# Performance work log

Measured on AMD Instinct MI355X. Metric: run time of the kernel, lower is better.

The kernel has to match this reference:

```python
import jax, jax.numpy as jnp
import numpy as np

B, S, D = 1, 2048, 1024
H, DK = 16, 64
DFF, E, K = 4096, 8, 2
EPS = float(np.finfo(np.float32).eps)  # torch nn.RMSNorm default eps = finfo.eps


def setup_inputs() -> dict:
    key = jax.random.key(0)
    ks = jax.random.split(key, 8)
    s = 0.02
    return {
        "x": jax.random.normal(ks[0], (B, S, D), jnp.float32),
        "qkv_w": jax.random.normal(ks[1], (3 * D, D), jnp.float32) * s,
        "out_w": jax.random.normal(ks[2], (D, D), jnp.float32) * s,
        "router_w": jax.random.normal(ks[3], (E, D), jnp.float32) * s,
        "w1": jax.random.normal(ks[4], (E, DFF, D), jnp.float32) * s,
        "w2": jax.random.normal(ks[5], (E, D, DFF), jnp.float32) * s,
        "norm1_w": jnp.ones((D,), jnp.float32),
        "norm2_w": jnp.ones((D,), jnp.float32),
    }


def _rmsnorm(x, w):
    return x * jax.lax.rsqrt(jnp.mean(x * x, axis=-1, keepdims=True) + EPS) * w


def _rope(x):
    # x: [B, S, H, dk]; rotate-half RoPE as in RotaryPositionalEmbedding
    dk = x.shape[-1]
    inv_freq = 1.0 / (10000.0 ** (jnp.arange(0, dk, 2, dtype=jnp.float32) / dk))
    t = jnp.arange(x.shape[1], dtype=jnp.float32)
    freqs = t[:, None] * inv_freq[None, :]          # [S, dk/2]
    cos = jnp.cos(freqs)[None, :, None, :]
    sin = jnp.sin(freqs)[None, :, None, :]
    x1, x2 = jnp.split(x, 2, axis=-1)
    return jnp.concatenate([x1 * cos - x2 * sin, x2 * cos + x1 * sin], axis=-1)


def _block(x, qkv_w, out_w, router_w, w1, w2, norm1_w, norm2_w):
    Bv, Sv, Dv = x.shape
    # --- attention with RoPE (causal, eval mode) ---
    h = _rmsnorm(x, norm1_w)
    qkv = (h @ qkv_w.T).reshape(Bv, Sv, 3, H, DK)
    q, k, v = qkv[:, :, 0], qkv[:, :, 1], qkv[:, :, 2]   # [B,S,H,dk]
    q = _rope(q)
    k = _rope(k)
    scores = jnp.einsum('bshd,bthd->bhst', q, k) / np.float32(np.sqrt(DK))
    causal = jnp.tril(jnp.ones((Sv, Sv), dtype=bool))
    scores = jnp.where(causal, scores, jnp.float32(-jnp.inf))
    attn = jax.nn.softmax(scores, axis=-1)
    o = jnp.einsum('bhst,bthd->bshd', attn, v).reshape(Bv, Sv, Dv)
    x = x + o @ out_w.T
    # --- MoE with top-k routing ---
    h2 = _rmsnorm(x, norm2_w).reshape(-1, Dv)            # [T, D]
    logits = h2 @ router_w.T                             # [T, E]
    probs = jax.nn.softmax(logits, axis=-1)
    top_p, top_i = jax.lax.top_k(probs, K)               # [T, K]
    top_p = top_p / jnp.sum(top_p, axis=-1, keepdims=True)
    T = h2.shape[0]
    # dense per-token per-expert combine weights (same math as masked loop)
    w_dense = jnp.zeros((T, E), h2.dtype).at[jnp.arange(T)[:, None], top_i].add(top_p)
    hid = jax.nn.gelu(jnp.einsum('td,efd->etf', h2, w1), approximate=False)  # [E,T,DFF]
    eo = jnp.einsum('etf,edf->etd', hid, w2)                                  # [E,T,D]
    moe = jnp.einsum('etd,te->td', eo, w_dense).reshape(Bv, Sv, Dv)
    aux_loss = E * jnp.sum(jnp.mean(probs, axis=0) ** 2)
    return x + moe, aux_loss


def reference(x, qkv_w, out_w, router_w, w1, w2, norm1_w, norm2_w):
    return _block(x, qkv_w, out_w, router_w, w1, w2, norm1_w, norm2_w)
```

## Files before the change

### kernel.cpp

```cpp
#include <hip/hip_runtime.h>
#include <cstdint>
#include <math.h>

typedef float f32x4 __attribute__((ext_vector_type(4)));
typedef __bf16 bf16x8 __attribute__((ext_vector_type(8)));
typedef unsigned short us4 __attribute__((ext_vector_type(4)));
typedef unsigned short us8 __attribute__((ext_vector_type(8)));

#define DEV static __device__ __forceinline__

DEV unsigned short f2bf(float f){
  union { __bf16 h; unsigned short u; } cv; cv.h = (__bf16)f; return cv.u;
}
DEV float bf2f(unsigned short u){ return __uint_as_float((unsigned int)u << 16); }

DEV void gload16(const void* g, void* l){
  __builtin_amdgcn_global_load_lds((__attribute__((address_space(1))) void*)g,
                                   (__attribute__((address_space(3))) void*)l, 16, 0, 0);
}

__global__ __launch_bounds__(256) void conv_kernel(const float* __restrict__ src,
    unsigned short* __restrict__ dst, int n8){
  int i = blockIdx.x*256 + threadIdx.x;
  if (i >= n8) return;
  float4 a = ((const float4*)src)[2*i];
  float4 b = ((const float4*)src)[2*i+1];
  us8 o = { f2bf(a.x), f2bf(a.y), f2bf(a.z), f2bf(a.w),
            f2bf(b.x), f2bf(b.y), f2bf(b.z), f2bf(b.w) };
  ((us8*)dst)[i] = o;
}

__global__ __launch_bounds__(256) void rmsnorm_kernel(const float* __restrict__ x, const float* __restrict__ w,
    unsigned short* __restrict__ ob){
  int t = blockIdx.x, tid = threadIdx.x;
  float4 xv = *(const float4*)(x + (long long)t*1024 + tid*4);
  float ss = xv.x*xv.x + xv.y*xv.y + xv.z*xv.z + xv.w*xv.w;
  for (int m=32;m;m>>=1) ss += __shfl_xor(ss,m);
  __shared__ float lds[4];
  if ((tid&63)==0) lds[tid>>6] = ss;
  __syncthreads();
  float tot = lds[0]+lds[1]+lds[2]+lds[3];
  float inv = rsqrtf(tot*(1.0f/1024.0f) + 1.1920928955078125e-07f);
  float4 wv = *(const float4*)(w + tid*4);
  us4 rb = { f2bf(xv.x*inv*wv.x), f2bf(xv.y*inv*wv.y), f2bf(xv.z*inv*wv.z), f2bf(xv.w*inv*wv.w) };
  *(us4*)&ob[(long long)t*1024 + tid*4] = rb;
}

__global__ __launch_bounds__(256) void rmsnorm2_kernel(const float* __restrict__ xp, int ksn, long long kstride,
    const float* __restrict__ w, float* __restrict__ x1, unsigned short* __restrict__ hb, float* __restrict__ hf){
  int t = blockIdx.x, tid = threadIdx.x;
  long long b = (long long)t*1024 + tid*4;
  float4 xv = {0.f,0.f,0.f,0.f};
  for (int ks=0; ks<ksn; ++ks){
    float4 a = *(const float4*)(xp + ks*kstride + b);
    xv.x+=a.x; xv.y+=a.y; xv.z+=a.z; xv.w+=a.w;
  }
  *(float4*)(x1 + b) = xv;
  float ss = xv.x*xv.x + xv.y*xv.y + xv.z*xv.z + xv.w*xv.w;
  for (int m=32;m;m>>=1) ss += __shfl_xor(ss,m);
  __shared__ float lds[4];
  if ((tid&63)==0) lds[tid>>6] = ss;
  __syncthreads();
  float tot = lds[0]+lds[1]+lds[2]+lds[3];
  float inv = rsqrtf(tot*(1.0f/1024.0f) + 1.1920928955078125e-07f);
  float4 wv = *(const float4*)(w + tid*4);
  float r0 = xv.x*inv*wv.x, r1 = xv.y*inv*wv.y, r2 = xv.z*inv*wv.z, r3 = xv.w*inv*wv.w;
  us4 rb = { f2bf(r0), f2bf(r1), f2bf(r2), f2bf(r3) };
  *(us4*)&hb[b] = rb;
  float4 rf; rf.x=r0; rf.y=r1; rf.z=r2; rf.w=r3;
  *(float4*)(hf + b) = rf;
}

template<int EPI, bool GATHER>
__global__ __launch_bounds__(256) void gemm_bb(
    const unsigned short* __restrict__ A, int lda,
    const unsigned short* __restrict__ Bb, long long bstride, int ldb,
    int M, int N, int K, int KS, long long ksoff,
    const int* __restrict__ counts, const int* __restrict__ offs,
    const int* __restrict__ tok_list, const float* __restrict__ wgt,
    const float* __restrict__ resid,
    float* __restrict__ Cf, unsigned short* __restrict__ Cb, int ldc)
{
  const int z = blockIdx.z;
  const int e = z / KS, ks = z - e*KS;
  const int Me = counts ? counts[e] : M;
  const int by = blockIdx.y;
  if (by * 128 >= Me) return;
  const int rbase = offs ? offs[e] : 0;
  const int bx = blockIdx.x;
  const unsigned short* B = Bb + (long long)e * bstride;
  const int kn = K / KS;
  const int kbeg = ks * kn;

  __shared__ __align__(16) unsigned short As[128*64];
  __shared__ __align__(16) unsigned short Bs[128*64];

  const int tid = threadIdx.x, lane = tid & 63, w = tid >> 6;
  const int wr = w >> 1, wc = w & 1;
  const int l15 = lane & 15, l4 = lane >> 4;

  const unsigned short* asrc[4];
  const unsigned short* bsrc[4];
  #pragma unroll
  for (int j=0;j<4;++j){
    int G = j*256 + tid;
    int R = G >> 3, c = G & 7;
    int sc = c ^ (R & 7);
    int lr = by*128 + R; if (lr >= Me) lr = Me-1;
    int li = rbase + lr;
    int ar = GATHER ? (tok_list[li] >> 1) : li;
    asrc[j] = A + (long long)ar*lda + kbeg + sc*8;
    bsrc[j] = B + (long long)(bx*128 + R)*ldb + kbeg + sc*8;
  }

  f32x4 acc[4][4] = {};

  for (int k0 = 0; k0 < kn; k0 += 64){
    __syncthreads();
    #pragma unroll
    for (int j=0;j<4;++j){
      gload16(asrc[j] + k0, &As[(j*256+tid)*8]);
      gload16(bsrc[j] + k0, &Bs[(j*256+tid)*8]);
    }
    __syncthreads();
    #pragma unroll
    for (int kk=0;kk<2;++kk){
      bf16x8 af[4], bfr[4];
      #pragma unroll
      for (int m=0;m<4;++m){
        int R = wr*64 + m*16 + l15;
        int c = (l4 + 4*kk) ^ (R&7);
        af[m] = *(const bf16x8*)&As[R*64 + c*8];
      }
      #pragma unroll
      for (int n=0;n<4;++n){
        int R = wc*64 + n*16 + l15;
        int c = (l4 + 4*kk) ^ (R&7);
        bfr[n] = *(const bf16x8*)&Bs[R*64 + c*8];
      }
      #pragma unroll
      for (int m=0;m<4;++m)
        #pragma unroll
        for (int n=0;n<4;++n)
          acc[m][n] = __builtin_amdgcn_mfma_f32_16x16x32_bf16(af[m], bfr[n], acc[m][n], 0, 0, 0);
    }
  }

  #pragma unroll
  for (int m=0;m<4;++m){
    #pragma unroll
    for (int r2=0;r2<4;++r2){
      int lr = by*128 + wr*64 + m*16 + 4*l4 + r2;
      if (lr >= Me) continue;
      #pragma unroll
      for (int n=0;n<4;++n){
        int col = bx*128 + wc*64 + n*16 + l15;
        float v = acc[m][n][r2];
        if constexpr (EPI == 1){
          if (ks == 0) v += resid[(long long)lr*ldc + col];
          Cf[ks*ksoff + (long long)lr*ldc + col] = v;
        } else if constexpr (EPI == 2){
          float g = 0.5f * v * (1.0f + erff(v * 0.70710678118654752f));
          Cb[(long long)(rbase+lr)*ldc + col] = f2bf(g);
        } else if constexpr (EPI == 3){
          int gi = rbase + lr;
          int ts = tok_list[gi];
          Cf[ks*ksoff + (long long)ts*ldc + col] = v * wgt[gi];
        } else {
          Cb[(long long)lr*ldc + col] = f2bf(v);
        }
      }
    }
  }
}

__global__ __launch_bounds__(256) void rope_kernel(const unsigned short* __restrict__ qkvb,
    unsigned short* __restrict__ q, unsigned short* __restrict__ k){
  int t = blockIdx.x, tid = threadIdx.x;
  const unsigned short* row = qkvb + (long long)t*3072;
  #pragma unroll
  for (int u2=0; u2<2; ++u2){
    int pid = tid + u2*256;
    int hh = pid >> 5, j = pid & 31;
    float invf = __expf(-(float)j * 0.28782313662425575f);
    float fr = (float)t * invf;
    float sn, cs;
    __sincosf(fr, &sn, &cs);
    int base = hh*64 + j;
    long long ob_ = (long long)t*1024 + base;
    float a = bf2f(row[base]), b = bf2f(row[base+32]);
    q[ob_]    = f2bf(a*cs - b*sn);
    q[ob_+32] = f2bf(b*cs + a*sn);
    a = bf2f(row[1024+base]); b = bf2f(row[1024+base+32]);
    k[ob_]    = f2bf(a*cs - b*sn);
    k[ob_+32] = f2bf(b*cs + a*sn);
  }
}

__global__ __launch_bounds__(256) void attn_kernel(
    const unsigned short* __restrict__ Q,
    const unsigned short* __restrict__ K,
    const unsigned short* __restrict__ V, int ldv,
    unsigned short* __restrict__ O)
{
  const int bx = blockIdx.x, h = blockIdx.y;
  const int q0 = bx*64;
  const int tid = threadIdx.x, lane = tid&63, w = tid>>6;

  __shared__ __align__(16) unsigned short Ks[64*64];
  __shared__ __align__(16) unsigned short Vs[64*64];
  __shared__ __align__(16) unsigned short Ps[4*16*64];
  unsigned short* Pw = Ps + w*1024;

  const int qrow = q0 + w*16 + (lane&15);
  bf16x8 aq[2];
  #pragma unroll
  for (int kk=0;kk<2;++kk)
    aq[kk] = *(const bf16x8*)&Q[(long long)qrow*1024 + h*64 + 32*kk + 8*(lane>>4)];

  f32x4 o[4] = {};
  float Mx[4] = {-INFINITY,-INFINITY,-INFINITY,-INFINITY};
  float Ls[4] = {0.f,0.f,0.f,0.f};

  const int row_g = q0 + w*16 + 4*(lane>>4);
  const int nt = bx + 1;
  for (int it = 0; it < nt; ++it){
    int k0 = it*64;
    #pragma unroll
    for (int i=0;i<2;++i){
      int seg = 4*i + w;
      int row = seg*8 + (lane>>3);
      int cs = (lane&7) ^ (row&7);
      gload16(&K[(long long)(k0+row)*1024 + h*64 + cs*8], &Ks[seg*512]);
      gload16(&V[(long long)(k0+row)*ldv  + h*64 + cs*8], &Vs[seg*512]);
    }
    __syncthreads();
    f32x4 st[4];
    #pragma unroll
    for (int kt=0;kt<4;++kt){
      f32x4 s = {0.f,0.f,0.f,0.f};
      #pragma unroll
      for (int kk=0;kk<2;++kk){
        int R = kt*16 + (lane&15);
        int ch = ((lane>>4)+4*kk) ^ (R&7);
        bf16x8 bk = *(const bf16x8*)&Ks[R*64 + ch*8];
        s = __builtin_amdgcn_mfma_f32_16x16x32_bf16(aq[kk], bk, s, 0,0,0);
      }
      st[kt] = s;
    }
    #pragma unroll
    for (int kt=0;kt<4;++kt){
      int col = k0 + kt*16 + (lane&15);
      #pragma unroll
      for (int r=0;r<4;++r){
        float vv = st[kt][r]*0.125f;
        st[kt][r] = (col <= row_g + r) ? vv : -INFINITY;
      }
    }
    float sf[4];
    #pragma unroll
    for (int r=0;r<4;++r){
      float mx = fmaxf(fmaxf(st[0][r],st[1][r]),fmaxf(st[2][r],st[3][r]));
      mx = fmaxf(mx, __shfl_xor(mx,1));
      mx = fmaxf(mx, __shfl_xor(mx,2));
      mx = fmaxf(mx, __shfl_xor(mx,4));
      mx = fmaxf(mx, __shfl_xor(mx,8));
      float mn = fmaxf(Mx[r], mx);
      float sc = __expf(Mx[r]-mn);
      Mx[r]=mn; sf[r]=sc;
      float ls=0.f;
      #pragma unroll
      for (int kt=0;kt<4;++kt){ float pp = __expf(st[kt][r]-mn); st[kt][r]=pp; ls+=pp; }
      Ls[r] = Ls[r]*sc + ls;
    }
    #pragma unroll
    for (int dt=0;dt<4;++dt)
      #pragma unroll
      for (int r=0;r<4;++r) o[dt][r] *= sf[r];
    #pragma unroll
    for (int kt=0;kt<4;++kt)
      #pragma unroll
      for (int r=0;r<4;++r){
        int prow = 4*(lane>>4)+r, pcol = kt*16+(lane&15);
        int byteoff = (prow*128 + pcol*2) ^ ((prow&7)<<4);
        *(unsigned short*)((char*)Pw + byteoff) = f2bf(st[kt][r]);
      }
    bf16x8 pa[2];
    #pragma unroll
    for (int kk=0;kk<2;++kk){
      int pr = lane&15;
      int ch = ((lane>>4)+4*kk) ^ (pr&7);
      pa[kk] = *(const bf16x8*)&Pw[pr*64 + ch*8];
    }
    #pragma unroll
    for (int dt=0;dt<4;++dt){
      #pragma unroll
      for (int kk=0;kk<2;++kk){
        union { unsigned short u[8]; bf16x8 v; } Ub;
        #pragma unroll
        for (int j=0;j<8;++j){
          int kr = 32*kk + 8*(lane>>4) + j;
          int d = dt*16 + (lane&15);
          int byteoff = (kr*128 + d*2) ^ ((kr&7)<<4);
          Ub.u[j] = *(const unsigned short*)((const char*)Vs + byteoff);
        }
        o[dt] = __builtin_amdgcn_mfma_f32_16x16x32_bf16(pa[kk], Ub.v, o[dt], 0,0,0);
      }
    }
    __syncthreads();
  }
  #pragma unroll
  for (int r=0;r<4;++r){
    float l = Ls[r];
    l += __shfl_xor(l,1); l += __shfl_xor(l,2); l += __shfl_xor(l,4); l += __shfl_xor(l,8);
    Ls[r] = 1.0f / l;
  }
  #pragma unroll
  for (int dt=0;dt<4;++dt)
    #pragma unroll
    for (int r=0;r<4;++r){
      float vv = o[dt][r]*Ls[r];
      int rg = row_g + r;
      O[(long long)rg*1024 + h*64 + dt*16 + (lane&15)] = f2bf(vv);
    }
}

__global__ __launch_bounds__(256) void router_kernel(const float* __restrict__ h2f, const float* __restrict__ rw,
    float* __restrict__ probs, int* __restrict__ tope, float* __restrict__ topw, int* __restrict__ counts){
  int t = blockIdx.x, tid = threadIdx.x;
  float4 hv = *(const float4*)(h2f + (long long)t*1024 + tid*4);
  float pe[8];
  #pragma unroll
  for (int e2=0;e2<8;++e2){
    float4 wv = *(const float4*)(rw + e2*1024 + tid*4);
    pe[e2] = hv.x*wv.x + hv.y*wv.y + hv.z*wv.z + hv.w*wv.w;
  }
  __shared__ float lds[32];
  #pragma unroll
  for (int e2=0;e2<8;++e2){
    float v = pe[e2];
    for (int m=32;m;m>>=1) v += __shfl_xor(v,m);
    if ((tid&63)==0) lds[(tid>>6)*8+e2] = v;
  }
  __syncthreads();
  if (tid==0){
    float lg[8], pp[8];
    #pragma unroll
    for (int e2=0;e2<8;++e2) lg[e2] = lds[e2]+lds[8+e2]+lds[16+e2]+lds[24+e2];
    float mx = lg[0];
    for (int e2=1;e2<8;++e2) mx = fmaxf(mx, lg[e2]);
    float s = 0.f;
    for (int e2=0;e2<8;++e2){ pp[e2] = __expf(lg[e2]-mx); s += pp[e2]; }
    float inv = 1.0f/s;
    int i0 = 0;
    for (int e2=1;e2<8;++e2) if (pp[e2] > pp[i0]) i0 = e2;
    int i1 = (i0==0)?1:0;
    for (int e2=0;e2<8;++e2) if (e2!=i0 && pp[e2] > pp[i1]) i1 = e2;
    for (int e2=0;e2<8;++e2) probs[t*8+e2] = pp[e2]*inv;
    float p0 = pp[i0], p1 = pp[i1], wsum = p0+p1;
    tope[t*2] = i0; tope[t*2+1] = i1;
    topw[t*2] = p0/wsum; topw[t*2+1] = p1/wsum;
    atomicAdd(&counts[i0],1); atomicAdd(&counts[i1],1);
  }
}

__global__ void init_kernel(int* counts, int* cursor){
  int i = threadIdx.x;
  if (i<8){ counts[i]=0; cursor[i]=0; }
}

__global__ void prefix_kernel(const int* counts, int* offs){
  if (threadIdx.x==0){
    int a=0;
    for (int e2=0;e2<8;++e2){ offs[e2]=a; a+=counts[e2]; }
  }
}

__global__ void scatter_kernel(const int* __restrict__ tope, const float* __restrict__ topw,
    const int* __restrict__ offs, int* __restrict__ cursor, int* __restrict__ tok_list, float* __restrict__ wgt){
  int t = blockIdx.x*blockDim.x + threadIdx.x;
  if (t >= 2048) return;
  #pragma unroll
  for (int s=0;s<2;++s){
    int e2 = tope[t*2+s];
    int pos = atomicAdd(&cursor[e2], 1);
    int i = offs[e2] + pos;
    tok_list[i] = t*2+s;
    wgt[i] = topw[t*2+s];
  }
}

__global__ __launch_bounds__(256) void aux_kernel(const float* __restrict__ probs, float* __restrict__ out){
  int tid = threadIdx.x;
  float pe[8] = {0,0,0,0,0,0,0,0};
  for (int t = tid; t < 2048; t += 256){
    #pragma unroll
    for (int e2=0;e2<8;++e2) pe[e2] += probs[t*8+e2];
  }
  __shared__ float lds[32];
  #pragma unroll
  for (int e2=0;e2<8;++e2){
    float v = pe[e2];
    for (int m=32;m;m>>=1) v += __shfl_xor(v,m);
    if ((tid&63)==0) lds[(tid>>6)*8 + e2] = v;
  }
  __syncthreads();
  if (tid==0){
    float aux = 0.f;
    #pragma unroll
    for (int e2=0;e2<8;++e2){
      float mean = (lds[e2]+lds[8+e2]+lds[16+e2]+lds[24+e2]) * (1.0f/2048.0f);
      aux += mean*mean;
    }
    out[2097152] = 8.0f * aux;
  }
}

__global__ __launch_bounds__(256) void final_kernel(const float* __restrict__ x1, const float* __restrict__ slots,
    int ksn, long long kstride, float* __restrict__ out){
  int t = blockIdx.x, tid = threadIdx.x;
  long long b = (long long)t*1024 + tid*4;
  float4 a = *(const float4*)(x1 + b);
  long long s = (long long)t*2048 + tid*4;
  for (int ks=0; ks<ksn; ++ks){
    float4 s0 = *(const float4*)(slots + ks*kstride + s);
    float4 s1 = *(const float4*)(slots + ks*kstride + s + 1024);
    a.x += s0.x + s1.x; a.y += s0.y + s1.y; a.z += s0.z + s1.z; a.w += s0.w + s1.w;
  }
  *(float4*)(out + b) = a;
}

extern "C" void kernel_launch(void* const* d_in, const int* in_sizes, int n_in,
                              void* d_out, int out_size, void* d_ws, size_t ws_size,
                              hipStream_t stream)
{
  (void)in_sizes; (void)n_in; (void)out_size; (void)ws_size;
  const float* x    = (const float*)d_in[0];
  const float* qkvw = (const float*)d_in[1];
  const float* outw = (const float*)d_in[2];
  const float* rw   = (const float*)d_in[3];
  const float* w1   = (const float*)d_in[4];
  const float* w2   = (const float*)d_in[5];
  const float* n1w  = (const float*)d_in[6];
  const float* n2w  = (const float*)d_in[7];
  float* out = (float*)d_out;

  char* base = (char*)d_ws;
  const size_t MB = 1ull<<20;
  const int KSO = 4;
  const int KSW = 2;

  unsigned short* h_b  = (unsigned short*)(base + 0*MB);
  unsigned short* qb   = (unsigned short*)(base + 4*MB);
  unsigned short* kb   = (unsigned short*)(base + 8*MB);
  unsigned short* ob   = (unsigned short*)(base + 12*MB);
  unsigned short* qkvb = (unsigned short*)(base + 16*MB);
  unsigned short* hid  = (unsigned short*)(base + 0*MB);

  unsigned short* wbq = (unsigned short*)(base + 32*MB);
  unsigned short* wbo = (unsigned short*)(base + 40*MB);
  unsigned short* wb  = (unsigned short*)(base + 32*MB);

  float* x1p   = (float*)(base + 96*MB);
  float* slots = (float*)(base + 96*MB);
  float* h2f   = (float*)(base + 128*MB);
  float* x1    = (float*)(base + 136*MB);
  unsigned short* h2b = (unsigned short*)(base + 144*MB);
  char* small_ = base + 148*MB;

  float* probs = (float*)(small_);
  int*   tope  = (int*)(small_ + 256*1024);
  float* topw  = (float*)(small_ + 512*1024);
  int*   tok_list = (int*)(small_ + 768*1024);
  float* wgt   = (float*)(small_ + 1024*1024);
  int*   counts= (int*)(small_ + 1536*1024);
  int*   offs  = (int*)(small_ + 1536*1024 + 256);
  int*   cursor= (int*)(small_ + 1536*1024 + 512);

  init_kernel<<<1,64,0,stream>>>(counts, cursor);
  rmsnorm_kernel<<<2048,256,0,stream>>>(x, n1w, h_b);
  conv_kernel<<<1536,256,0,stream>>>(qkvw, wbq, 3*1024*1024/8);
  conv_kernel<<<512,256,0,stream>>>(outw, wbo, 1024*1024/8);
  gemm_bb<4,false><<<dim3(24,16,1),256,0,stream>>>(h_b,1024, wbq,0,1024, 2048,3072,1024, 1,0,
      nullptr,nullptr,nullptr,nullptr,nullptr, nullptr,qkvb,3072);
  rope_kernel<<<2048,256,0,stream>>>(qkvb, qb, kb);
  attn_kernel<<<dim3(32,16),256,0,stream>>>(qb, kb, qkvb+2048, 3072, ob);
  gemm_bb<1,false><<<dim3(8,16,KSO),256,0,stream>>>(ob,1024, wbo,0,1024, 2048,1024,1024, KSO,(long long)2048*1024,
      nullptr,nullptr,nullptr,nullptr, x, x1p,nullptr,1024);
  rmsnorm2_kernel<<<2048,256,0,stream>>>(x1p, KSO, (long long)2048*1024, n2w, x1, h2b, h2f);
  router_kernel<<<2048,256,0,stream>>>(h2f, rw, probs, tope, topw, counts);
  prefix_kernel<<<1,64,0,stream>>>(counts, offs);
  scatter_kernel<<<8,256,0,stream>>>(tope, topw, offs, cursor, tok_list, wgt);
  conv_kernel<<<16384,256,0,stream>>>(w1, wb, 32*1024*1024/8);
  gemm_bb<2,true><<<dim3(32,16,8),256,0,stream>>>(h2b,1024, wb,(long long)4096*1024,1024, 2048,4096,1024, 1,0,
      counts,offs,tok_list,nullptr,nullptr, nullptr,hid,4096);
  conv_kernel<<<16384,256,0,stream>>>(w2, wb, 32*1024*1024/8);
  gemm_bb<3,false><<<dim3(8,16,8*KSW),256,0,stream>>>(hid,4096, wb,(long long)4096*1024,4096, 2048,1024,4096, KSW,(long long)4096*1024,
      counts,offs,tok_list,wgt,nullptr, slots,nullptr,1024);
  aux_kernel<<<1,256,0,stream>>>(probs, out);
  final_kernel<<<2048,256,0,stream>>>(x1, slots, KSW, (long long)4096*1024, out);
}
```

Measured before the change: 436.5 us.

## Pre-transpose V for attention and schedule longest causal query blocks first

```diff
diff --git a/kernel.cpp b/kernel.cpp
--- a/kernel.cpp
+++ b/kernel.cpp
@@ -28,6 +28,26 @@
   us8 o = { f2bf(a.x), f2bf(a.y), f2bf(a.z), f2bf(a.w),
             f2bf(b.x), f2bf(b.y), f2bf(b.z), f2bf(b.w) };
   ((us8*)dst)[i] = o;
+}
+
+__global__ __launch_bounds__(256) void vtrans_kernel(const unsigned short* __restrict__ qkvb,
+    unsigned short* __restrict__ vt){
+  int tt = blockIdx.x, h = blockIdx.y;
+  int t0 = tt*64;
+  __shared__ unsigned short tile[64][72];
+  int r = threadIdx.x >> 2, cb = (threadIdx.x & 3) * 16;
+  const unsigned short* src = qkvb + (long long)(t0+r)*3072 + 2048 + h*64 + cb;
+  us8 a = *(const us8*)src;
+  us8 b = *(const us8*)(src+8);
+  #pragma unroll
+  for (int i=0;i<8;++i){ tile[r][cb+i] = a[i]; tile[r][cb+8+i] = b[i]; }
+  __syncthreads();
+  unsigned short o[16];
+  #pragma unroll
+  for (int i=0;i<16;++i) o[i] = tile[cb+i][r];
+  unsigned short* dst = vt + (long long)(h*64+r)*2048 + t0 + cb;
+  *(us8*)dst = *(us8*)&o[0];
+  *(us8*)(dst+8) = *(us8*)&o[8];
 }
 
 __global__ __launch_bounds__(256) void rmsnorm_kernel(const float* __restrict__ x, const float* __restrict__ w,
@@ -200,29 +220,31 @@
 __global__ __launch_bounds__(256) void attn_kernel(
     const unsigned short* __restrict__ Q,
     const unsigned short* __restrict__ K,
-    const unsigned short* __restrict__ V, int ldv,
+    const unsigned short* __restrict__ Vt,
     unsigned short* __restrict__ O)
 {
-  const int bx = blockIdx.x, h = blockIdx.y;
+  const int bx = gridDim.x - 1 - blockIdx.x;
+  const int h = blockIdx.y;
   const int q0 = bx*64;
   const int tid = threadIdx.x, lane = tid&63, w = tid>>6;
+  const int l15 = lane & 15, l4 = lane >> 4;
 
   __shared__ __align__(16) unsigned short Ks[64*64];
   __shared__ __align__(16) unsigned short Vs[64*64];
   __shared__ __align__(16) unsigned short Ps[4*16*64];
   unsigned short* Pw = Ps + w*1024;
 
-  const int qrow = q0 + w*16 + (lane&15);
+  const int qrow = q0 + w*16 + l15;
   bf16x8 aq[2];
   #pragma unroll
   for (int kk=0;kk<2;++kk)
-    aq[kk] = *(const bf16x8*)&Q[(long long)qrow*1024 + h*64 + 32*kk + 8*(lane>>4)];
+    aq[kk] = *(const bf16x8*)&Q[(long long)qrow*1024 + h*64 + 32*kk + 8*l4];
 
   f32x4 o[4] = {};
   float Mx[4] = {-INFINITY,-INFINITY,-INFINITY,-INFINITY};
   float Ls[4] = {0.f,0.f,0.f,0.f};
 
-  const int row_g = q0 + w*16 + 4*(lane>>4);
+  const int row_g = q0 + w*16 + 4*l4;
   const int nt = bx + 1;
   for (int it = 0; it < nt; ++it){
     int k0 = it*64;
@@ -232,7 +254,7 @@
       int row = seg*8 + (lane>>3);
       int cs = (lane&7) ^ (row&7);
       gload16(&K[(long long)(k0+row)*1024 + h*64 + cs*8], &Ks[seg*512]);
-      gload16(&V[(long long)(k0+row)*ldv  + h*64 + cs*8], &Vs[seg*512]);
+      gload16(&Vt[(long long)(h*64+row)*2048 + k0 + cs*8], &Vs[seg*512]);
     }
     __syncthreads();
     f32x4 st[4];
@@ -241,8 +263,8 @@
       f32x4 s = {0.f,0.f,0.f,0.f};
       #pragma unroll
       for (int kk=0;kk<2;++kk){
-        int R = kt*16 + (lane&15);
-        int ch = ((lane>>4)+4*kk) ^ (R&7);
+        int R = kt*16 + l15;
+        int ch = (l4+4*kk) ^ (R&7);
         bf16x8 bk = *(const bf16x8*)&Ks[R*64 + ch*8];
         s = __builtin_amdgcn_mfma_f32_16x16x32_bf16(aq[kk], bk, s, 0,0,0);
       }
@@ -250,7 +272,7 @@
     }
     #pragma unroll
     for (int kt=0;kt<4;++kt){
-      int col = k0 + kt*16 + (lane&15);
+      int col = k0 + kt*16 + l15;
       #pragma unroll
       for (int r=0;r<4;++r){
         float vv = st[kt][r]*0.125f;
@@ -281,30 +303,25 @@
     for (int kt=0;kt<4;++kt)
       #pragma unroll
       for (int r=0;r<4;++r){
-        int prow = 4*(lane>>4)+r, pcol = kt*16+(lane&15);
+        int prow = 4*l4+r, pcol = kt*16+l15;
         int byteoff = (prow*128 + pcol*2) ^ ((prow&7)<<4);
         *(unsigned short*)((char*)Pw + byteoff) = f2bf(st[kt][r]);
       }
     bf16x8 pa[2];
     #pragma unroll
     for (int kk=0;kk<2;++kk){
-      int pr = lane&15;
-      int ch = ((lane>>4)+4*kk) ^ (pr&7);
+      int pr = l15;
+      int ch = (l4+4*kk) ^ (pr&7);
       pa[kk] = *(const bf16x8*)&Pw[pr*64 + ch*8];
     }
     #pragma unroll
     for (int dt=0;dt<4;++dt){
       #pragma unroll
       for (int kk=0;kk<2;++kk){
-        union { unsigned short u[8]; bf16x8 v; } Ub;
-        #pragma unroll
-        for (int j=0;j<8;++j){
-          int kr = 32*kk + 8*(lane>>4) + j;
-          int d = dt*16 + (lane&15);
-          int byteoff = (kr*128 + d*2) ^ ((kr&7)<<4);
-          Ub.u[j] = *(const unsigned short*)((const char*)Vs + byteoff);
-        }
-        o[dt] = __builtin_amdgcn_mfma_f32_16x16x32_bf16(pa[kk], Ub.v, o[dt], 0,0,0);
+        int R = dt*16 + l15;
+        int c = (l4 + 4*kk) ^ (R&7);
+        bf16x8 bv = *(const bf16x8*)&Vs[R*64 + c*8];
+        o[dt] = __builtin_amdgcn_mfma_f32_16x16x32_bf16(pa[kk], bv, o[dt], 0,0,0);
       }
     }
     __syncthreads();
@@ -321,7 +338,7 @@
     for (int r=0;r<4;++r){
       float vv = o[dt][r]*Ls[r];
       int rg = row_g + r;
-      O[(long long)rg*1024 + h*64 + dt*16 + (lane&15)] = f2bf(vv);
+      O[(long long)rg*1024 + h*64 + dt*16 + l15] = f2bf(vv);
     }
 }
 
@@ -455,6 +472,7 @@
   unsigned short* kb   = (unsigned short*)(base + 8*MB);
   unsigned short* ob   = (unsigned short*)(base + 12*MB);
   unsigned short* qkvb = (unsigned short*)(base + 16*MB);
+  unsigned short* vt   = (unsigned short*)(base + 28*MB);
   unsigned short* hid  = (unsigned short*)(base + 0*MB);
 
   unsigned short* wbq = (unsigned short*)(base + 32*MB);
@@ -484,7 +502,8 @@
   gemm_bb<4,false><<<dim3(24,16,1),256,0,stream>>>(h_b,1024, wbq,0,1024, 2048,3072,1024, 1,0,
       nullptr,nullptr,nullptr,nullptr,nullptr, nullptr,qkvb,3072);
   rope_kernel<<<2048,256,0,stream>>>(qkvb, qb, kb);
-  attn_kernel<<<dim3(32,16),256,0,stream>>>(qb, kb, qkvb+2048, 3072, ob);
+  vtrans_kernel<<<dim3(32,16),256,0,stream>>>(qkvb, vt);
+  attn_kernel<<<dim3(32,16),256,0,stream>>>(qb, kb, vt, ob);
   gemm_bb<1,false><<<dim3(8,16,KSO),256,0,stream>>>(ob,1024, wbo,0,1024, 2048,1024,1024, KSO,(long long)2048*1024,
       nullptr,nullptr,nullptr,nullptr, x, x1p,nullptr,1024);
   rmsnorm2_kernel<<<2048,256,0,stream>>>(x1p, KSO, (long long)2048*1024, n2w, x1, h2b, h2f);
```

Measured after the change: 419.0 us. -4.0%, faster.
